# Kernel tuning notes

Hardware: AMD Instinct MI355X
Metric: run time of the kernel (lower is better)

Reference implementation:

```python
import jax, jax.numpy as jnp
import numpy as np

B, N, V, H = 8, 2048, 256, 1024
EPS = 1e-5
NEG = -1e9


def _layernorm(x, g, b):
    m = jnp.mean(x, axis=-1, keepdims=True)
    v = jnp.mean((x - m) ** 2, axis=-1, keepdims=True)
    return (x - m) / jnp.sqrt(v + EPS) * g + b


def setup_inputs() -> dict:
    key = jax.random.key(0)
    ks = jax.random.split(key, 10)
    tril = jnp.tril(jnp.ones((N, N), jnp.float32))
    return {
        "h": jax.random.normal(ks[0], (B, N, V), jnp.float32),
        "mask_one": tril,                      # keep causal entries
        "mask_zero": NEG * (1.0 - tril),       # -inf-ish above diagonal
        "ln_attn_g": jnp.ones((V,), jnp.float32),
        "ln_attn_b": jnp.zeros((V,), jnp.float32),
        "ln_mlp_g": jnp.ones((V,), jnp.float32),
        "ln_mlp_b": jnp.zeros((V,), jnp.float32),
        "wv": jax.random.normal(ks[1], (V,), jnp.float32),
        "wv_bos": jax.random.normal(ks[2], (V,), jnp.float32),
        "wo_w": jax.random.normal(ks[3], (V, V), jnp.float32) / np.sqrt(V),
        "qk_bos": jax.random.normal(ks[4], (V,), jnp.float32),
        "qk_previous": jax.random.normal(ks[5], (V,), jnp.float32),
        "qk_direction": jnp.ones((V,), jnp.float32),  # middel_layer=False, frozen
        "w1": jax.random.normal(ks[6], (H, V), jnp.float32) / np.sqrt(V),
        "w2": jax.random.normal(ks[7], (V, H), jnp.float32) / np.sqrt(H),
    }


def reference(h, mask_one, mask_zero, ln_attn_g, ln_attn_b, ln_mlp_g, ln_mlp_b,
              wv, wv_bos, wo_w, qk_bos, qk_previous, qk_direction, w1, w2):
    b, n, v = h.shape
    # mask blends LayerNorm only into row 0 (BOS position)
    attn_input = h.at[:, 0, :].set(_layernorm(h[:, 0, :], ln_attn_g, ln_attn_b))
    # value states: diag(wv) on positions 1.., wo(wv_bos) at position 0
    values = attn_input[:, 1:, :] * wv                      # [B, N-1, V]
    v_bos = wo_w @ wv_bos                                   # Linear(bias=False)
    values = jnp.concatenate(
        [jnp.broadcast_to(v_bos, (b, 1, v)), values], axis=1)  # [B, N, V]
    # sparse QK logits: column 0 term + sub-diagonal term, densified then masked
    col0 = (attn_input @ qk_bos) * (attn_input[:, 0, :] @ qk_direction)[:, None]  # [B, N]
    d = attn_input @ qk_previous                            # [B, N]
    qk = jnp.zeros((b, n, n), h.dtype).at[:, :, 0].add(col0)
    idx = jnp.arange(1, n)
    qk = qk.at[:, idx, idx - 1].add(d[:, 1:])               # row r, col r-1 = d[:, r]
    qk = qk * mask_one + mask_zero
    attn_out = jax.nn.softmax(qk, axis=-1) @ values         # [B, N, V]
    # FFN branch with its own BOS-only LayerNorm blend
    mlp_input = h.at[:, 0, :].set(_layernorm(h[:, 0, :], ln_mlp_g, ln_mlp_b))
    mlp_out = jax.nn.relu(mlp_input @ w1.T) @ w2.T          # [B, N, V]
    return attn_out + mlp_out
```

## Files before the change

kernel.cpp:

```cpp
#include <hip/hip_runtime.h>
#include <hip/hip_bf16.h>

#define BB 8
#define NN 2048
#define VV 256
#define HH 1024
#define CHK 64
#define RPC 32
constexpr float EPS = 1e-5f;

typedef __attribute__((ext_vector_type(4))) float floatx4;
typedef __attribute__((ext_vector_type(8))) short short8;

__device__ __forceinline__ void load_lds16(const void* g, void* l) {
    __builtin_amdgcn_global_load_lds((const __attribute__((address_space(1))) void*)g,
                                     (__attribute__((address_space(3))) void*)l, 16, 0, 0);
}
__device__ __forceinline__ float bf16s_to_f(short s) {
    unsigned u = ((unsigned)(unsigned short)s) << 16;
    return __builtin_bit_cast(float, u);
}

__global__ void prep_kernel(const float* __restrict__ h,
                            const float* __restrict__ g_attn, const float* __restrict__ b_attn,
                            const float* __restrict__ g_mlp,  const float* __restrict__ b_mlp,
                            const float* __restrict__ qk_dir,
                            const float* __restrict__ wo_w,  const float* __restrict__ wv_bos,
                            float* __restrict__ attn_row0, float* __restrict__ mlp_row0,
                            float* __restrict__ v_bos, float* __restrict__ sum0)
{
    int t = threadIdx.x;
    __shared__ float red[VV];
    if (blockIdx.x < BB) {
        int b = blockIdx.x;
        float x = h[(size_t)b * NN * VV + t];
        red[t] = x; __syncthreads();
        for (int s = 128; s > 0; s >>= 1) { if (t < s) red[t] += red[t + s]; __syncthreads(); }
        float m = red[0] * (1.0f / VV); __syncthreads();
        float xc = x - m;
        red[t] = xc * xc; __syncthreads();
        for (int s = 128; s > 0; s >>= 1) { if (t < s) red[t] += red[t + s]; __syncthreads(); }
        float var = red[0] * (1.0f / VV); __syncthreads();
        float inv = 1.0f / sqrtf(var + EPS);
        float an = xc * inv * g_attn[t] + b_attn[t];
        float mn = xc * inv * g_mlp[t] + b_mlp[t];
        attn_row0[b * VV + t] = an;
        mlp_row0[b * VV + t]  = mn;
        red[t] = an * qk_dir[t]; __syncthreads();
        for (int s = 128; s > 0; s >>= 1) { if (t < s) red[t] += red[t + s]; __syncthreads(); }
        if (t == 0) sum0[b] = red[0];
    } else {
        const float4* wp = reinterpret_cast<const float4*>(wo_w + (size_t)t * VV);
        const float4* vp = reinterpret_cast<const float4*>(wv_bos);
        float acc = 0.f;
        for (int j = 0; j < VV / 4; ++j) {
            float4 a = wp[j], b = vp[j];
            acc += a.x * b.x + a.y * b.y + a.z * b.z + a.w * b.w;
        }
        v_bos[t] = acc;
    }
}

__global__ __launch_bounds__(256) void scan_qkw_cvt_kernel(
    const float* __restrict__ h, const float* __restrict__ mlp_row0,
    const float* __restrict__ wv,
    const float* __restrict__ qk_bos, const float* __restrict__ qk_prev,
    const float* __restrict__ sum0,
    short* __restrict__ Xb,
    float* __restrict__ w0, float* __restrict__ wprev, float* __restrict__ wz,
    float* __restrict__ chunkSum)
{
    __shared__ float lds[4][VV];
    int wave = threadIdx.x >> 6, lane = threadIdx.x & 63;
    int b = blockIdx.x / CHK, c = blockIdx.x % CHK;
    int r0 = c * RPC + wave * 8;
    float4 wv4 = reinterpret_cast<const float4*>(wv)[lane];
    float4 qb4 = reinterpret_cast<const float4*>(qk_bos)[lane];
    float4 qp4 = reinterpret_cast<const float4*>(qk_prev)[lane];
    float s0b = sum0[b];
    float4 vsum = {0.f, 0.f, 0.f, 0.f};
#pragma unroll
    for (int rr = 0; rr < 8; ++rr) {
        int r = r0 + rr;
        size_t base = ((size_t)b * NN + r) * VV;
        float4 x = *reinterpret_cast<const float4*>(h + base + lane * 4);
        float4 xs = x;
        if (r == 0) xs = *reinterpret_cast<const float4*>(mlp_row0 + b * VV + lane * 4);
        __hip_bfloat16 c0 = __float2bfloat16(xs.x), c1 = __float2bfloat16(xs.y),
                       c2 = __float2bfloat16(xs.z), c3 = __float2bfloat16(xs.w);
        short4 pk;
        pk.x = *reinterpret_cast<short*>(&c0);
        pk.y = *reinterpret_cast<short*>(&c1);
        pk.z = *reinterpret_cast<short*>(&c2);
        pk.w = *reinterpret_cast<short*>(&c3);
        *reinterpret_cast<short4*>(Xb + base + lane * 4) = pk;
        if (r != 0) {
            vsum.x += bf16s_to_f(pk.x) * wv4.x; vsum.y += bf16s_to_f(pk.y) * wv4.y;
            vsum.z += bf16s_to_f(pk.z) * wv4.z; vsum.w += bf16s_to_f(pk.w) * wv4.w;
        }
        float s1 = x.x * qb4.x + x.y * qb4.y + x.z * qb4.z + x.w * qb4.w;
        float s2 = x.x * qp4.x + x.y * qp4.y + x.z * qp4.z + x.w * qp4.w;
        for (int off = 32; off > 0; off >>= 1) {
            s1 += __shfl_down(s1, off);
            s2 += __shfl_down(s2, off);
        }
        if (lane == 0) {
            int gid = b * NN + r;
            float W0, WP, WZ;
            if (r == 0) { W0 = 1.f; WP = 0.f; WZ = 0.f; }
            else if (r == 1) {
                float a = s1 * s0b + s2;
                float m = fmaxf(a, 0.f);
                float ea = expf(a - m), ez = expf(-m);
                float Z = ea + ez;
                W0 = ea / Z; WZ = ez / Z; WP = WZ;
            } else {
                float a = s1 * s0b;
                float m = fmaxf(fmaxf(a, s2), 0.f);
                float ea = expf(a - m), ed = expf(s2 - m), ez = expf(-m);
                float Z = ea + ed + (float)(r - 1) * ez;
                W0 = ea / Z; WP = ed / Z; WZ = ez / Z;
            }
            w0[gid] = W0; wprev[gid] = WP; wz[gid] = WZ;
        }
    }
    reinterpret_cast<float4*>(lds[wave])[lane] = vsum;
    __syncthreads();
    int v = threadIdx.x;
    chunkSum[((size_t)b * CHK + c) * VV + v] = lds[0][v] + lds[1][v] + lds[2][v] + lds[3][v];
}

__global__ void chunkscan_kernel(float* __restrict__ chunkSum)
{
    int b = blockIdx.x, v = threadIdx.x;
    float vals[CHK];
#pragma unroll
    for (int c = 0; c < CHK; ++c) vals[c] = chunkSum[(b * CHK + c) * VV + v];
    float run = 0.f;
#pragma unroll
    for (int c = 0; c < CHK; ++c) { float t = vals[c]; vals[c] = run; run += t; }
#pragma unroll
    for (int c = 0; c < CHK; ++c) chunkSum[(b * CHK + c) * VV + v] = vals[c];
}

__global__ __launch_bounds__(128) void attn_kernel(
    const short* __restrict__ Xb, const float* __restrict__ wv,
    const float* __restrict__ v_bos,
    const float* __restrict__ w0, const float* __restrict__ wprev,
    const float* __restrict__ wz, const float* __restrict__ chunkSum,
    float* __restrict__ out)
{
    int b = blockIdx.x / CHK, c = blockIdx.x % CHK;
    int v = threadIdx.x * 2;
    float2 wv2 = *reinterpret_cast<const float2*>(wv + v);
    float2 vb2 = *reinterpret_cast<const float2*>(v_bos + v);
    float2 S = *reinterpret_cast<const float2*>(chunkSum + (b * CHK + c) * VV + v);
    int r0 = c * RPC;
    float2 prev = {0.f, 0.f};
    if (r0 > 0) {
        short2 p = *reinterpret_cast<const short2*>(Xb + ((size_t)b * NN + r0 - 1) * VV + v);
        prev.x = bf16s_to_f(p.x) * wv2.x; prev.y = bf16s_to_f(p.y) * wv2.y;
    }
    for (int r = r0; r < r0 + RPC; ++r) {
        size_t idx = ((size_t)b * NN + r) * VV + v;
        float2 o;
        if (r == 0) {
            o = vb2;
            prev.x = 0.f; prev.y = 0.f;
        } else {
            short2 xv = *reinterpret_cast<const short2*>(Xb + idx);
            float2 val;
            val.x = bf16s_to_f(xv.x) * wv2.x; val.y = bf16s_to_f(xv.y) * wv2.y;
            S.x += val.x; S.y += val.y;
            int wi = b * NN + r;
            float W0 = w0[wi], WD = wprev[wi] - wz[wi], WZ = wz[wi];
            o.x = W0 * vb2.x + WD * prev.x + WZ * S.x;
            o.y = W0 * vb2.y + WD * prev.y + WZ * S.y;
            prev = val;
        }
        *reinterpret_cast<float2*>(out + idx) = o;
    }
}

__global__ void cvt_w_kernel(const float* __restrict__ w1, const float* __restrict__ w2,
                             __hip_bfloat16* __restrict__ w1b, __hip_bfloat16* __restrict__ w2b)
{
    int i = (blockIdx.x * blockDim.x + threadIdx.x) * 4;
    const float* src;
    __hip_bfloat16* dst;
    if (i < HH * VV) { src = w1 + i; dst = w1b + i; }
    else             { src = w2 + (i - HH * VV); dst = w2b + (i - HH * VV); }
    float4 x = *reinterpret_cast<const float4*>(src);
    dst[0] = __float2bfloat16(x.x);
    dst[1] = __float2bfloat16(x.y);
    dst[2] = __float2bfloat16(x.z);
    dst[3] = __float2bfloat16(x.w);
}

__global__ __launch_bounds__(512) void mlp_fused3(const short* __restrict__ Xb,
                                                  const short* __restrict__ w1b,
                                                  const short* __restrict__ w2b,
                                                  float* __restrict__ out)
{
    __shared__ __align__(16) short sW1[2][64 * 256];
    __shared__ __align__(16) short sW2[2][256 * 64];
    __shared__ __align__(16) short sY[64 * 64];
    int wave = threadIdx.x >> 6, lane = threadIdx.x & 63;
    int wm = wave >> 2, wn = wave & 3;
    int ra = lane & 15, q = lane >> 4;
    int m0 = blockIdx.x * 64;

    short8 xf[8][2];
#pragma unroll
    for (int ks = 0; ks < 8; ++ks)
#pragma unroll
        for (int i = 0; i < 2; ++i)
            xf[ks][i] = *reinterpret_cast<const short8*>(
                Xb + (size_t)(m0 + wm * 32 + i * 16 + ra) * VV + ks * 32 + q * 8);

    floatx4 oacc[2][4];
#pragma unroll
    for (int i = 0; i < 2; ++i)
#pragma unroll
        for (int j = 0; j < 4; ++j) oacc[i][j] = floatx4{0.f, 0.f, 0.f, 0.f};

    auto stage = [&](int hc, int buf) {
#pragma unroll
        for (int it = 0; it < 4; ++it) {
            int g = wave * 4 + it;
            int n = g * 2 + (lane >> 5);
            int slot = lane & 31;
            load_lds16(w1b + (size_t)(hc * 64 + n) * VV + (slot ^ (n & 7)) * 8,
                       &sW1[buf][g * 512]);
        }
#pragma unroll
        for (int it = 0; it < 4; ++it) {
            int g = wave * 4 + it;
            int v = g * 8 + (lane >> 3);
            int slot = lane & 7;
            load_lds16(w2b + (size_t)v * HH + hc * 64 + (slot ^ (v & 7)) * 8,
                       &sW2[buf][g * 512]);
        }
    };

    stage(0, 0);
    for (int hc = 0; hc < 16; ++hc) {
        int p = hc & 1;
        __syncthreads();
        if (hc < 15) stage(hc + 1, p ^ 1);

        floatx4 yacc[2];
        yacc[0] = floatx4{0.f, 0.f, 0.f, 0.f};
        yacc[1] = floatx4{0.f, 0.f, 0.f, 0.f};
        int nb = wn * 16 + ra;
#pragma unroll
        for (int ks = 0; ks < 8; ++ks) {
            short8 bfr = *reinterpret_cast<const short8*>(
                &sW1[p][nb * 256 + (((ks * 4 + q) ^ (ra & 7)) * 8)]);
#pragma unroll
            for (int i = 0; i < 2; ++i)
                yacc[i] = __builtin_amdgcn_mfma_f32_16x16x32_bf16(xf[ks][i], bfr, yacc[i], 0, 0, 0);
        }
#pragma unroll
        for (int i = 0; i < 2; ++i)
#pragma unroll
            for (int reg = 0; reg < 4; ++reg) {
                int m = wm * 32 + i * 16 + q * 4 + reg;
                int ke = wn * 16 + ra;
                __hip_bfloat16 hb = __float2bfloat16(fmaxf(yacc[i][reg], 0.f));
                sY[m * 64 + (((ke >> 3) ^ (m & 7)) * 8) + (ke & 7)] =
                    *reinterpret_cast<short*>(&hb);
            }
        __syncthreads();

#pragma unroll
        for (int kk = 0; kk < 2; ++kk) {
            short8 a2[2];
#pragma unroll
            for (int i = 0; i < 2; ++i) {
                int m = wm * 32 + i * 16 + ra;
                a2[i] = *reinterpret_cast<const short8*>(
                    &sY[m * 64 + (((kk * 4 + q) ^ (ra & 7)) * 8)]);
            }
#pragma unroll
            for (int j = 0; j < 4; ++j) {
                int v = wn * 64 + j * 16 + ra;
                short8 b2 = *reinterpret_cast<const short8*>(
                    &sW2[p][v * 64 + (((kk * 4 + q) ^ (ra & 7)) * 8)]);
#pragma unroll
                for (int i = 0; i < 2; ++i)
                    oacc[i][j] = __builtin_amdgcn_mfma_f32_16x16x32_bf16(a2[i], b2, oacc[i][j], 0, 0, 0);
            }
        }
    }

#pragma unroll
    for (int i = 0; i < 2; ++i)
#pragma unroll
        for (int j = 0; j < 4; ++j)
#pragma unroll
            for (int reg = 0; reg < 4; ++reg) {
                int row = m0 + wm * 32 + i * 16 + q * 4 + reg;
                int col = wn * 64 + j * 16 + ra;
                out[(size_t)row * VV + col] += oacc[i][j][reg];
            }
}

extern "C" void kernel_launch(void* const* d_in, const int* in_sizes, int n_in,
                              void* d_out, int out_size, void* d_ws, size_t ws_size,
                              hipStream_t stream)
{
    const float* h        = (const float*)d_in[0];
    const float* ln_attn_g = (const float*)d_in[3];
    const float* ln_attn_b = (const float*)d_in[4];
    const float* ln_mlp_g  = (const float*)d_in[5];
    const float* ln_mlp_b  = (const float*)d_in[6];
    const float* wv        = (const float*)d_in[7];
    const float* wv_bos    = (const float*)d_in[8];
    const float* wo_w      = (const float*)d_in[9];
    const float* qk_bos    = (const float*)d_in[10];
    const float* qk_prev   = (const float*)d_in[11];
    const float* qk_dir    = (const float*)d_in[12];
    const float* w1        = (const float*)d_in[13];
    const float* w2        = (const float*)d_in[14];
    float* out = (float*)d_out;

    float* attn_row0 = (float*)d_ws;
    float* mlp_row0  = attn_row0 + BB * VV;
    float* v_bos     = mlp_row0 + BB * VV;
    float* sum0      = v_bos + VV;
    float* w0        = sum0 + 8;
    float* wprev     = w0 + BB * NN;
    float* wzz       = wprev + BB * NN;
    float* chunkSum  = wzz + BB * NN;
    short* Xb            = (short*)(chunkSum + BB * CHK * VV);
    __hip_bfloat16* w1b  = (__hip_bfloat16*)(Xb + (size_t)BB * NN * VV);
    __hip_bfloat16* w2b  = w1b + HH * VV;

    prep_kernel<<<BB + 1, 256, 0, stream>>>(h, ln_attn_g, ln_attn_b, ln_mlp_g, ln_mlp_b,
                                            qk_dir, wo_w, wv_bos,
                                            attn_row0, mlp_row0, v_bos, sum0);
    cvt_w_kernel<<<(2 * HH * VV / 4) / 256, 256, 0, stream>>>(w1, w2, w1b, w2b);
    scan_qkw_cvt_kernel<<<BB * CHK, 256, 0, stream>>>(h, mlp_row0, wv, qk_bos, qk_prev,
                                                      sum0, Xb, w0, wprev, wzz, chunkSum);
    chunkscan_kernel<<<BB, 256, 0, stream>>>(chunkSum);
    attn_kernel<<<BB * CHK, 128, 0, stream>>>(Xb, wv, v_bos, w0, wprev, wzz, chunkSum, out);
    mlp_fused3<<<256, 512, 0, stream>>>(Xb, (const short*)w1b, (const short*)w2b, out);
}
```

Measured before the change: 173.0 us.

## Fuse attention epilogue into MLP kernel and weight conversion into scan kernel

Removes the separate attention kernel and weight-conversion kernel. The attention recurrence now runs as an epilogue of the MLP GEMM, which stages its output tile in LDS and adds the attention result before a single store. This removes the read-modify-write of the output buffer and two launches. The per-row softmax weights are packed into one float4, and the bf16 weight cast is folded into the scan kernel's blocks. In exchange the MLP kernel grows its shared memory to 136 KB and gains a serial per-row tail.

```diff
diff --git a/kernel.cpp b/kernel.cpp
--- a/kernel.cpp
+++ b/kernel.cpp
@@ -67,8 +67,10 @@
     const float* __restrict__ qk_bos, const float* __restrict__ qk_prev,
     const float* __restrict__ sum0,
     short* __restrict__ Xb,
-    float* __restrict__ w0, float* __restrict__ wprev, float* __restrict__ wz,
-    float* __restrict__ chunkSum)
+    float* __restrict__ wpack,
+    float* __restrict__ chunkSum,
+    const float* __restrict__ w1, const float* __restrict__ w2,
+    short* __restrict__ w1b, short* __restrict__ w2b)
 {
     __shared__ float lds[4][VV];
     int wave = threadIdx.x >> 6, lane = threadIdx.x & 63;
@@ -121,10 +123,29 @@
                 float Z = ea + ed + (float)(r - 1) * ez;
                 W0 = ea / Z; WP = ed / Z; WZ = ez / Z;
             }
-            w0[gid] = W0; wprev[gid] = WP; wz[gid] = WZ;
+            float4 wp4 = {W0, WP - WZ, WZ, 0.f};
+            *reinterpret_cast<float4*>(wpack + (size_t)gid * 4) = wp4;
         }
     }
     reinterpret_cast<float4*>(lds[wave])[lane] = vsum;
+
+    {
+        int gi = blockIdx.x * 256 + threadIdx.x;
+        size_t off = (size_t)gi * 4;
+        const float* src; short* dst;
+        if (off < (size_t)HH * VV) { src = w1 + off; dst = w1b + off; }
+        else                       { src = w2 + (off - (size_t)HH * VV); dst = w2b + (off - (size_t)HH * VV); }
+        float4 x = *reinterpret_cast<const float4*>(src);
+        __hip_bfloat16 c0 = __float2bfloat16(x.x), c1 = __float2bfloat16(x.y),
+                       c2 = __float2bfloat16(x.z), c3 = __float2bfloat16(x.w);
+        short4 pk;
+        pk.x = *reinterpret_cast<short*>(&c0);
+        pk.y = *reinterpret_cast<short*>(&c1);
+        pk.z = *reinterpret_cast<short*>(&c2);
+        pk.w = *reinterpret_cast<short*>(&c3);
+        *reinterpret_cast<short4*>(dst) = pk;
+    }
+
     __syncthreads();
     int v = threadIdx.x;
     chunkSum[((size_t)b * CHK + c) * VV + v] = lds[0][v] + lds[1][v] + lds[2][v] + lds[3][v];
@@ -143,68 +164,20 @@
     for (int c = 0; c < CHK; ++c) chunkSum[(b * CHK + c) * VV + v] = vals[c];
 }
 
-__global__ __launch_bounds__(128) void attn_kernel(
-    const short* __restrict__ Xb, const float* __restrict__ wv,
-    const float* __restrict__ v_bos,
-    const float* __restrict__ w0, const float* __restrict__ wprev,
-    const float* __restrict__ wz, const float* __restrict__ chunkSum,
-    float* __restrict__ out)
-{
-    int b = blockIdx.x / CHK, c = blockIdx.x % CHK;
-    int v = threadIdx.x * 2;
-    float2 wv2 = *reinterpret_cast<const float2*>(wv + v);
-    float2 vb2 = *reinterpret_cast<const float2*>(v_bos + v);
-    float2 S = *reinterpret_cast<const float2*>(chunkSum + (b * CHK + c) * VV + v);
-    int r0 = c * RPC;
-    float2 prev = {0.f, 0.f};
-    if (r0 > 0) {
-        short2 p = *reinterpret_cast<const short2*>(Xb + ((size_t)b * NN + r0 - 1) * VV + v);
-        prev.x = bf16s_to_f(p.x) * wv2.x; prev.y = bf16s_to_f(p.y) * wv2.y;
-    }
-    for (int r = r0; r < r0 + RPC; ++r) {
-        size_t idx = ((size_t)b * NN + r) * VV + v;
-        float2 o;
-        if (r == 0) {
-            o = vb2;
-            prev.x = 0.f; prev.y = 0.f;
-        } else {
-            short2 xv = *reinterpret_cast<const short2*>(Xb + idx);
-            float2 val;
-            val.x = bf16s_to_f(xv.x) * wv2.x; val.y = bf16s_to_f(xv.y) * wv2.y;
-            S.x += val.x; S.y += val.y;
-            int wi = b * NN + r;
-            float W0 = w0[wi], WD = wprev[wi] - wz[wi], WZ = wz[wi];
-            o.x = W0 * vb2.x + WD * prev.x + WZ * S.x;
-            o.y = W0 * vb2.y + WD * prev.y + WZ * S.y;
-            prev = val;
-        }
-        *reinterpret_cast<float2*>(out + idx) = o;
-    }
-}
-
-__global__ void cvt_w_kernel(const float* __restrict__ w1, const float* __restrict__ w2,
-                             __hip_bfloat16* __restrict__ w1b, __hip_bfloat16* __restrict__ w2b)
-{
-    int i = (blockIdx.x * blockDim.x + threadIdx.x) * 4;
-    const float* src;
-    __hip_bfloat16* dst;
-    if (i < HH * VV) { src = w1 + i; dst = w1b + i; }
-    else             { src = w2 + (i - HH * VV); dst = w2b + (i - HH * VV); }
-    float4 x = *reinterpret_cast<const float4*>(src);
-    dst[0] = __float2bfloat16(x.x);
-    dst[1] = __float2bfloat16(x.y);
-    dst[2] = __float2bfloat16(x.z);
-    dst[3] = __float2bfloat16(x.w);
-}
-
-__global__ __launch_bounds__(512) void mlp_fused3(const short* __restrict__ Xb,
+__global__ __launch_bounds__(512) void mlp_fused4(const short* __restrict__ Xb,
                                                   const short* __restrict__ w1b,
                                                   const short* __restrict__ w2b,
+                                                  const float* __restrict__ wv,
+                                                  const float* __restrict__ v_bos,
+                                                  const float* __restrict__ wpack,
+                                                  const float* __restrict__ chunkSum,
                                                   float* __restrict__ out)
 {
-    __shared__ __align__(16) short sW1[2][64 * 256];
-    __shared__ __align__(16) short sW2[2][256 * 64];
-    __shared__ __align__(16) short sY[64 * 64];
+    __shared__ __align__(16) char smem[136 * 1024];
+    short (*sW1)[64 * 256] = reinterpret_cast<short(*)[64 * 256]>(smem);
+    short (*sW2)[256 * 64] = reinterpret_cast<short(*)[256 * 64]>(smem + 65536);
+    short* sY = reinterpret_cast<short*>(smem + 131072);
+
     int wave = threadIdx.x >> 6, lane = threadIdx.x & 63;
     int wm = wave >> 2, wn = wave & 3;
     int ra = lane & 15, q = lane >> 4;
@@ -294,16 +267,49 @@
         }
     }
 
+    __syncthreads();
+    float* sOut = reinterpret_cast<float*>(smem);
 #pragma unroll
     for (int i = 0; i < 2; ++i)
 #pragma unroll
         for (int j = 0; j < 4; ++j)
 #pragma unroll
             for (int reg = 0; reg < 4; ++reg) {
-                int row = m0 + wm * 32 + i * 16 + q * 4 + reg;
+                int l = wm * 32 + i * 16 + q * 4 + reg;
                 int col = wn * 64 + j * 16 + ra;
-                out[(size_t)row * VV + col] += oacc[i][j][reg];
-            }
+                sOut[l * 260 + col] = oacc[i][j][reg];
+            }
+    __syncthreads();
+
+    {
+        int v    = threadIdx.x & 255;
+        int half = threadIdx.x >> 8;
+        int b  = m0 >> 11;
+        int n0 = m0 & (NN - 1);
+        int r0 = n0 + half * RPC;
+        float wvv = wv[v];
+        float vb  = v_bos[v];
+        float S = chunkSum[((size_t)b * CHK + (r0 >> 5)) * VV + v];
+        float prev = 0.f;
+        int r = r0;
+        if (r0 == 0) {
+            out[((size_t)b * NN) * VV + v] = vb + sOut[0 * 260 + v];
+            r = 1;
+        } else {
+            short p = Xb[((size_t)b * NN + r0 - 1) * VV + v];
+            prev = bf16s_to_f(p) * wvv;
+        }
+#pragma unroll 4
+        for (; r < r0 + RPC; ++r) {
+            size_t idx = ((size_t)b * NN + r) * VV + v;
+            float val = bf16s_to_f(Xb[idx]) * wvv;
+            S += val;
+            float4 wp4 = *reinterpret_cast<const float4*>(wpack + (size_t)(b * NN + r) * 4);
+            float o = wp4.x * vb + wp4.y * prev + wp4.z * S;
+            prev = val;
+            out[idx] = o + sOut[(r - n0) * 260 + v];
+        }
+    }
 }
 
 extern "C" void kernel_launch(void* const* d_in, const int* in_sizes, int n_in,
@@ -329,21 +335,18 @@
     float* mlp_row0  = attn_row0 + BB * VV;
     float* v_bos     = mlp_row0 + BB * VV;
     float* sum0      = v_bos + VV;
-    float* w0        = sum0 + 8;
-    float* wprev     = w0 + BB * NN;
-    float* wzz       = wprev + BB * NN;
-    float* chunkSum  = wzz + BB * NN;
-    short* Xb            = (short*)(chunkSum + BB * CHK * VV);
-    __hip_bfloat16* w1b  = (__hip_bfloat16*)(Xb + (size_t)BB * NN * VV);
-    __hip_bfloat16* w2b  = w1b + HH * VV;
+    float* wpack     = sum0 + 8;
+    float* chunkSum  = wpack + (size_t)BB * NN * 4;
+    short* Xb        = (short*)(chunkSum + BB * CHK * VV);
+    short* w1b       = (short*)(Xb + (size_t)BB * NN * VV);
+    short* w2b       = w1b + HH * VV;
 
     prep_kernel<<<BB + 1, 256, 0, stream>>>(h, ln_attn_g, ln_attn_b, ln_mlp_g, ln_mlp_b,
                                             qk_dir, wo_w, wv_bos,
                                             attn_row0, mlp_row0, v_bos, sum0);
-    cvt_w_kernel<<<(2 * HH * VV / 4) / 256, 256, 0, stream>>>(w1, w2, w1b, w2b);
     scan_qkw_cvt_kernel<<<BB * CHK, 256, 0, stream>>>(h, mlp_row0, wv, qk_bos, qk_prev,
-                                                      sum0, Xb, w0, wprev, wzz, chunkSum);
+                                                      sum0, Xb, wpack, chunkSum,
+                                                      w1, w2, w1b, w2b);
     chunkscan_kernel<<<BB, 256, 0, stream>>>(chunkSum);
-    attn_kernel<<<BB * CHK, 128, 0, stream>>>(Xb, wv, v_bos, w0, wprev, wzz, chunkSum, out);
-    mlp_fused3<<<256, 512, 0, stream>>>(Xb, (const short*)w1b, (const short*)w2b, out);
-}
+    mlp_fused4<<<256, 512, 0, stream>>>(Xb, w1b, w2b, wv, v_bos, wpack, chunkSum, out);
+}
```

Result: faster. 163.1 us (-5.7%).
